# Kernel optimization log

Hardware: AMD Instinct MI355X
Metric: run time of the kernel (lower is better)

Reference implementation:

```python
import jax, jax.numpy as jnp
import numpy as np

DIM = 1024
N_HEADS = 16
HEAD_DIM = DIM // N_HEADS
B, T = 4, 2048


def setup_inputs() -> dict:
    key = jax.random.key(0)
    k_x, k_cos, k_sin, k_wqkv, k_wout = jax.random.split(key, 5)
    x = jax.random.normal(k_x, (B, T, DIM), dtype=jnp.float32)
    # rotary tables indexed by position, half the head dim
    pos = jnp.arange(T, dtype=jnp.float32)[:, None]
    inv_freq = 1.0 / (10000.0 ** (jnp.arange(0, HEAD_DIM, 2, dtype=jnp.float32) / HEAD_DIM))
    ang = pos * inv_freq[None, :]  # [T, HEAD_DIM//2]
    cos = jnp.cos(ang)
    sin = jnp.sin(ang)
    mask = jnp.zeros((T, T), dtype=jnp.float32)
    Wqkv = jax.random.normal(k_wqkv, (3 * DIM, DIM), dtype=jnp.float32) * 0.02
    Wout = jax.random.normal(k_wout, (DIM, DIM), dtype=jnp.float32) * 0.02
    return {"x": x, "cos": cos, "sin": sin, "mask": mask, "Wqkv": Wqkv, "Wout": Wout}


def _apply_rope(t, cos, sin):
    # t: [B, T, H, D]; cos/sin: [T, D//2]
    d = t.shape[-1]
    t1, t2 = t[..., : d // 2], t[..., d // 2 :]
    c = cos[: t.shape[1]][None, :, None, :]
    s = sin[: t.shape[1]][None, :, None, :]
    return jnp.concatenate([t1 * c - t2 * s, t1 * s + t2 * c], axis=-1)


def reference(x, cos, sin, mask, Wqkv, Wout):
    Bx, Tx, C = x.shape
    scale = HEAD_DIM ** -0.5
    qkv = (x @ Wqkv.T).reshape(Bx, Tx, 3, N_HEADS, HEAD_DIM)
    q, k, v = qkv[:, :, 0], qkv[:, :, 1], qkv[:, :, 2]
    q = _apply_rope(q, cos, sin)
    k = _apply_rope(k, cos, sin)
    attn = jnp.einsum("bthd,bshd->bhts", q, k) * scale  # [B, H, T, T]
    attn = attn + mask[None, None, :, :]
    p = jax.nn.softmax(attn, axis=-1)
    out = jnp.einsum("bhts,bshd->bthd", p, v).reshape(Bx, Tx, C)
    return out @ Wout.T
```

## Files before the change

### kernel.cpp

```cpp
#include <hip/hip_runtime.h>
#include <math.h>

#define DIMC   1024
#define NHEADS 16
#define HD     64
#define BATCH  4
#define SEQ    2048
#define MROWS  (BATCH * SEQ)
#define QKVC   (3 * DIMC)
#define QSCALE 0.1803368801111204f

typedef __bf16 bf16x8 __attribute__((ext_vector_type(8)));
typedef float  f32x4  __attribute__((ext_vector_type(4)));
typedef short  s16x4  __attribute__((ext_vector_type(4)));
typedef unsigned short us;

#define MFMA16(a, b, c) __builtin_amdgcn_mfma_f32_16x16x32_bf16(a, b, c, 0, 0, 0)

__device__ __forceinline__ f32x4 mfma16x16x16(s16x4 a, s16x4 b, f32x4 c) {
#if __has_builtin(__builtin_amdgcn_mfma_f32_16x16x16bf16_1k)
    return __builtin_amdgcn_mfma_f32_16x16x16bf16_1k(a, b, c, 0, 0, 0);
#else
    asm volatile("v_mfma_f32_16x16x16_bf16 %0, %1, %2, %0"
                 : "+v"(c) : "v"(a), "v"(b));
    return c;
#endif
}

__device__ __forceinline__ void async16(const void* g, void* l) {
    __builtin_amdgcn_global_load_lds(
        (const __attribute__((address_space(1))) void*)g,
        (__attribute__((address_space(3))) void*)l, 16, 0, 0);
}

__device__ __forceinline__ bf16x8 ldsfrag(const us* p) {
    union { int4 q; bf16x8 v; } u;
    u.q = *(const int4*)p;
    return u.v;
}

__device__ __forceinline__ s16x4 ldsfrag64(const us* p) {
    union { uint2 q; s16x4 v; } u;
    u.q = *(const uint2*)p;
    return u.v;
}

__device__ __forceinline__ bf16x8 gfrag(const us* __restrict__ p) {
    union { int4 q; bf16x8 v; } u;
    u.q = *(const int4*)p;
    return u.v;
}

__device__ __forceinline__ us bf16_rn(float f) {
    unsigned int u = __builtin_bit_cast(unsigned int, f);
    u += 0x7fffu + ((u >> 16) & 1u);
    return (us)(u >> 16);
}

__device__ __forceinline__ float fast_exp2(float x) {
#if __has_builtin(__builtin_amdgcn_exp2f)
    return __builtin_amdgcn_exp2f(x);
#else
    return __expf(x * 0.6931471805599453f);
#endif
}

__device__ __forceinline__ s16x4 pack4t(float a, float b, float c, float d) {
    union { unsigned u[2]; s16x4 v; } z;
    z.u[0] = __builtin_amdgcn_perm(__builtin_bit_cast(unsigned, b),
                                   __builtin_bit_cast(unsigned, a), 0x07060302);
    z.u[1] = __builtin_amdgcn_perm(__builtin_bit_cast(unsigned, d),
                                   __builtin_bit_cast(unsigned, c), 0x07060302);
    return z.v;
}

#define NX (MROWS * DIMC)
#define NW (QKVC * DIMC)
#define NO (DIMC * DIMC)
#define NC (SEQ * 32)
__global__ __launch_bounds__(256) void cast3_bf16(const float* __restrict__ x,
                                                  const float* __restrict__ wq,
                                                  const float* __restrict__ wo,
                                                  const float* __restrict__ cosb,
                                                  const float* __restrict__ sinb,
                                                  us* __restrict__ xb,
                                                  us* __restrict__ wqb,
                                                  us* __restrict__ wob,
                                                  float* __restrict__ cs2) {
    int i = (blockIdx.x * 256 + threadIdx.x) * 4;
    const float* src;
    us* dst;
    if (i < NX)                { src = x  + i;             dst = xb  + i; }
    else if (i < NX + NW)      { src = wq + (i - NX);      dst = wqb + (i - NX); }
    else if (i < NX + NW + NO) { src = wo + (i - NX - NW); dst = wob + (i - NX - NW); }
    else {
        int p0 = i - (NX + NW + NO);
        if (p0 >= NC) return;
        float4 c4 = *(const float4*)(cosb + p0);
        float4 s4 = *(const float4*)(sinb + p0);
        float4 o0 = {c4.x, s4.x, c4.y, s4.y};
        float4 o1 = {c4.z, s4.z, c4.w, s4.w};
        *(float4*)(cs2 + 2 * p0)     = o0;
        *(float4*)(cs2 + 2 * p0 + 4) = o1;
        return;
    }
    float4 v = *(const float4*)src;
    ushort4 o = {bf16_rn(v.x), bf16_rn(v.y), bf16_rn(v.z), bf16_rn(v.w)};
    *(ushort4*)dst = o;
}

template <int MODE, int NCOLS, int NBLK>
__global__ __launch_bounds__(512, 1) void gemm256(const us* __restrict__ A,
                                                  const us* __restrict__ B,
                                                  void* __restrict__ Cv,
                                                  const float* __restrict__ cs2,
                                                  us* __restrict__ vt) {
    __shared__ __align__(16) us As[3][256 * 64];
    __shared__ __align__(16) us Bs[3][128 * 64];

    const int tid  = threadIdx.x;
    const int lane = tid & 63, w = tid >> 6;
    const int col  = lane & 15, quad = lane >> 4;
    const int r8   = lane >> 3, c8 = lane & 7;
    const int wm   = (w >> 1) * 64, wn = (w & 1) * 64;

    const int f    = blockIdx.y * gridDim.x + blockIdx.x;
    const int xcd  = f & 7, idx = f >> 3;
    const int m0   = (xcd * 4 + idx / NBLK) * 256;
    const int n0   = (idx % NBLK) * 128;

    const us* Ag = A + (size_t)(m0 + w * 8 + r8) * 1024 + (c8 ^ r8) * 8;
    const us* Bg = B + (size_t)(n0 + w * 8 + r8) * 1024 + (c8 ^ r8) * 8;
    us* Ad = &As[0][0] + w * 512 + lane * 8;
    us* Bd = &Bs[0][0] + w * 512 + lane * 8;

    auto stage0 = [&](int kt, int bb) __attribute__((always_inline)) {
        const us* ag = Ag + kt * 64;
        us* ad = Ad + bb * (256 * 64);
        async16(ag, ad);
        async16(ag + (size_t)64 * 1024, ad + 4096);
        async16(Bg + kt * 64, Bd + bb * (128 * 64));
    };
    auto stage1 = [&](int kt, int bb) __attribute__((always_inline)) {
        const us* ag = Ag + kt * 64;
        us* ad = Ad + bb * (256 * 64);
        async16(ag + (size_t)128 * 1024, ad + 8192);
        async16(ag + (size_t)192 * 1024, ad + 12288);
        async16(Bg + kt * 64 + (size_t)64 * 1024, Bd + bb * (128 * 64) + 4096);
    };

    f32x4 acc[4][4] = {};

    stage0(0, 0); stage1(0, 0);
    stage0(1, 1); stage1(1, 1);
    asm volatile("s_waitcnt vmcnt(6)" ::: "memory");
    __builtin_amdgcn_s_barrier();
    __builtin_amdgcn_sched_barrier(0);

    const int swz = col & 7;
#pragma unroll
    for (int kt = 0; kt < 16; ++kt) {
        const us* Ab = &As[kt % 3][0];
        const us* Bb = &Bs[kt % 3][0];
        const int nb = (kt + 2) % 3;
        const bool pf = (kt + 2 < 16);

        {
            bf16x8 af[4], bf[4];
#pragma unroll
            for (int mt = 0; mt < 4; ++mt)
                af[mt] = ldsfrag(Ab + (wm + mt * 16 + col) * 64 + ((quad ^ swz) * 8));
#pragma unroll
            for (int nt = 0; nt < 4; ++nt)
                bf[nt] = ldsfrag(Bb + (wn + nt * 16 + col) * 64 + ((quad ^ swz) * 8));
            if (pf) stage0(kt + 2, nb);
            __builtin_amdgcn_s_barrier();
            asm volatile("s_waitcnt lgkmcnt(0)" ::: "memory");
            __builtin_amdgcn_sched_barrier(0);
            __builtin_amdgcn_s_setprio(1);
#pragma unroll
            for (int mt = 0; mt < 4; ++mt)
#pragma unroll
                for (int nt = 0; nt < 4; ++nt)
                    acc[mt][nt] = MFMA16(af[mt], bf[nt], acc[mt][nt]);
            __builtin_amdgcn_s_setprio(0);
            __builtin_amdgcn_s_barrier();
        }
        {
            bf16x8 af[4], bf[4];
#pragma unroll
            for (int mt = 0; mt < 4; ++mt)
                af[mt] = ldsfrag(Ab + (wm + mt * 16 + col) * 64 + (((4 + quad) ^ swz) * 8));
#pragma unroll
            for (int nt = 0; nt < 4; ++nt)
                bf[nt] = ldsfrag(Bb + (wn + nt * 16 + col) * 64 + (((4 + quad) ^ swz) * 8));
            if (pf) stage1(kt + 2, nb);
            __builtin_amdgcn_s_barrier();
            asm volatile("s_waitcnt lgkmcnt(0)" ::: "memory");
            __builtin_amdgcn_sched_barrier(0);
            __builtin_amdgcn_s_setprio(1);
#pragma unroll
            for (int mt = 0; mt < 4; ++mt)
#pragma unroll
                for (int nt = 0; nt < 4; ++nt)
                    acc[mt][nt] = MFMA16(af[mt], bf[nt], acc[mt][nt]);
            __builtin_amdgcn_s_setprio(0);
            if (kt + 2 < 16)
                asm volatile("s_waitcnt vmcnt(6)" ::: "memory");
            else if (kt + 1 < 16)
                asm volatile("s_waitcnt vmcnt(0)" ::: "memory");
            __builtin_amdgcn_s_barrier();
            __builtin_amdgcn_sched_barrier(0);
        }
    }

    if constexpr (MODE == 1) {
        us* C = (us*)Cv;
        const int gcol0 = n0 + wn;
        const bool is_v = (gcol0 >= 2 * DIMC);
        if (is_v) {
            const int hh   = (gcol0 - 2 * DIMC) >> 6;
            const int bidx = (m0 + wm) >> 11;
            const int tb0  = (m0 + wm) & (SEQ - 1);
#pragma unroll
            for (int mt = 0; mt < 4; ++mt) {
                const int tb = tb0 + mt * 16 + quad * 4;
#pragma unroll
                for (int nt = 0; nt < 4; ++nt) {
                    const int d = nt * 16 + col;
                    ushort4 o = {bf16_rn(acc[mt][nt][0]), bf16_rn(acc[mt][nt][1]),
                                 bf16_rn(acc[mt][nt][2]), bf16_rn(acc[mt][nt][3])};
                    *(ushort4*)(vt + ((size_t)((bidx * 16 + hh) * 64 + d)) * SEQ + tb) = o;
                }
            }
        } else {
            const float fq = (gcol0 < DIMC) ? QSCALE : 1.0f;
#pragma unroll
            for (int mt = 0; mt < 4; ++mt) {
#pragma unroll
                for (int r = 0; r < 4; ++r) {
                    const int grow = m0 + wm + mt * 16 + quad * 4 + r;
                    const int t = grow & (SEQ - 1);
#pragma unroll
                    for (int nt = 0; nt < 2; ++nt) {
                        const int d1 = nt * 16 + col;
                        const float2 cs = ((const float2*)cs2)[t * 32 + d1];
                        const float v1 = acc[mt][nt][r];
                        const float v2 = acc[mt][nt + 2][r];
                        C[(size_t)grow * NCOLS + gcol0 + d1]      = bf16_rn((v1 * cs.x - v2 * cs.y) * fq);
                        C[(size_t)grow * NCOLS + gcol0 + d1 + 32] = bf16_rn((v1 * cs.y + v2 * cs.x) * fq);
                    }
                }
            }
        }
    } else {
        float* C = (float*)Cv;
#pragma unroll
        for (int mt = 0; mt < 4; ++mt)
#pragma unroll
            for (int nt = 0; nt < 4; ++nt)
#pragma unroll
                for (int r = 0; r < 4; ++r)
                    C[(size_t)(m0 + wm + mt * 16 + quad * 4 + r) * NCOLS +
                      n0 + wn + nt * 16 + col] = acc[mt][nt][r];
    }
}

__global__ __launch_bounds__(256, 2) void attn_mfma(const us* __restrict__ qkv,
                                                    const us* __restrict__ vt,
                                                    us* __restrict__ outb) {
    __shared__ __align__(16) us Ls[4][8192];

    const int tid  = threadIdx.x;
    const int lane = tid & 63, w = tid >> 6;
    const int col  = lane & 15, quad = lane >> 4;

    const int f  = blockIdx.y * gridDim.x + blockIdx.x;
    const int c  = (f & 7) * 64 + (f >> 3);
    const int bh = c >> 3, b = bh >> 4, h = bh & 15;
    const int t0 = (c & 7) * 256;

    const int r8 = lane >> 3;
    const int cs = ((lane & 7) ^ r8) * 8;

    const int sw0 = ((quad ^ (col & 7)) << 3);
    const int sw4 = sw0 ^ 32;
    const int e2 = quad >> 1, o4 = (quad & 1) * 4, cm = col & 7;

    const us* qb = qkv + (size_t)b * SEQ * QKVC + h * HD;

    bf16x8 aq[4][2];
#pragma unroll
    for (int s = 0; s < 4; ++s)
#pragma unroll
        for (int hf = 0; hf < 2; ++hf)
            aq[s][hf] = gfrag(qb + (size_t)(t0 + s * 64 + w * 16 + col) * QKVC +
                              hf * 32 + quad * 8);

    const us* kg0 = qkv + (size_t)(b * SEQ + r8) * QKVC + DIMC + h * HD + cs;
    const us* vg0 = vt + ((size_t)bh * HD + r8) * SEQ + cs;
    us* kl = &Ls[w][0]    + lane * 8;
    us* vl = &Ls[w][4096] + lane * 8;

    union { us u[4]; s16x4 v; } ones4;
#pragma unroll
    for (int i = 0; i < 4; ++i) ones4.u[i] = 0x3F80;

    f32x4 o_acc[4][4] = {};
    f32x4 lacc[4] = {};

#pragma unroll
    for (int i = 0; i < 8; ++i)
        async16(kg0 + (size_t)(8 * i) * QKVC, kl + 512 * i);
#pragma unroll
    for (int i = 0; i < 8; ++i)
        async16(vg0 + (size_t)(8 * i) * SEQ, vl + 512 * i);
    asm volatile("s_waitcnt vmcnt(0)" ::: "memory");
    __builtin_amdgcn_sched_barrier(0);

    for (int s0 = 0; s0 < SEQ; s0 += 64) {
        const us* Kb = &Ls[w][0];
        const us* Vb = &Ls[w][4096];

        bf16x8 bk[4][2];
        s16x4  bv[4][4];
#pragma unroll
        for (int nt = 0; nt < 4; ++nt) {
            bk[nt][0] = ldsfrag(Kb + (nt * 16 + col) * 64 + sw0);
            bk[nt][1] = ldsfrag(Kb + (nt * 16 + col) * 64 + sw4);
#pragma unroll
            for (int dt = 0; dt < 4; ++dt)
                bv[nt][dt] = ldsfrag64(Vb + (dt * 16 + col) * 64 +
                                       (((nt * 2 + e2) ^ cm) << 3) + o4);
        }
        asm volatile("s_waitcnt lgkmcnt(0)" ::: "memory");
        __builtin_amdgcn_sched_barrier(0);

        if (s0 + 64 < SEQ) {
            const us* kn = kg0 + (size_t)(s0 + 64) * QKVC;
            const us* vn = vg0 + (s0 + 64);
#pragma unroll
            for (int i = 0; i < 8; ++i)
                async16(kn + (size_t)(8 * i) * QKVC, kl + 512 * i);
#pragma unroll
            for (int i = 0; i < 8; ++i)
                async16(vn + (size_t)(8 * i) * SEQ, vl + 512 * i);
        }

#pragma unroll
        for (int s = 0; s < 4; ++s) {
            f32x4 st[4] = {};
            __builtin_amdgcn_s_setprio(1);
#pragma unroll
            for (int nt = 0; nt < 4; ++nt) {
                st[nt] = MFMA16(bk[nt][0], aq[s][0], st[nt]);
                st[nt] = MFMA16(bk[nt][1], aq[s][1], st[nt]);
            }
            __builtin_amdgcn_s_setprio(0);
            s16x4 ap[4];
#pragma unroll
            for (int nt = 0; nt < 4; ++nt)
                ap[nt] = pack4t(fast_exp2(st[nt][0]), fast_exp2(st[nt][1]),
                                fast_exp2(st[nt][2]), fast_exp2(st[nt][3]));
            __builtin_amdgcn_s_setprio(1);
#pragma unroll
            for (int nt = 0; nt < 4; ++nt)
                lacc[s] = mfma16x16x16(ap[nt], ones4.v, lacc[s]);
#pragma unroll
            for (int dt = 0; dt < 4; ++dt)
#pragma unroll
                for (int nt = 0; nt < 4; ++nt)
                    o_acc[s][dt] = mfma16x16x16(ap[nt], bv[nt][dt], o_acc[s][dt]);
            __builtin_amdgcn_s_setprio(0);
        }

        if (s0 + 64 < SEQ) {
            asm volatile("s_waitcnt vmcnt(0)" ::: "memory");
            __builtin_amdgcn_sched_barrier(0);
        }
    }

#pragma unroll
    for (int s = 0; s < 4; ++s) {
        float linv[4];
#pragma unroll
        for (int r = 0; r < 4; ++r) linv[r] = __builtin_amdgcn_rcpf(lacc[s][r]);
#pragma unroll
        for (int dt = 0; dt < 4; ++dt)
#pragma unroll
            for (int r = 0; r < 4; ++r) {
                const int t = t0 + s * 64 + w * 16 + quad * 4 + r;
                const int d = h * HD + dt * 16 + col;
                outb[(size_t)(b * SEQ + t) * DIMC + d] = bf16_rn(o_acc[s][dt][r] * linv[r]);
            }
    }
}

extern "C" void kernel_launch(void* const* d_in, const int* in_sizes, int n_in,
                              void* d_out, int out_size, void* d_ws, size_t ws_size,
                              hipStream_t stream) {
    const float* x    = (const float*)d_in[0];
    const float* cosb = (const float*)d_in[1];
    const float* sinb = (const float*)d_in[2];
    const float* Wqkv = (const float*)d_in[4];
    const float* Wout = (const float*)d_in[5];
    float* out = (float*)d_out;

    us* xb    = (us*)d_ws;
    us* wqkb  = xb + (size_t)MROWS * DIMC;
    us* woutb = wqkb + (size_t)QKVC * DIMC;
    us* qkvb  = woutb + (size_t)DIMC * DIMC;
    us* vtb   = qkvb + (size_t)MROWS * QKVC;
    us* aob   = vtb + (size_t)BATCH * NHEADS * HD * SEQ;
    float* cs2 = (float*)(aob + (size_t)MROWS * DIMC);

    cast3_bf16<<<(NX + NW + NO + NC) / 1024, 256, 0, stream>>>(
        x, Wqkv, Wout, cosb, sinb, xb, wqkb, woutb, cs2);

    gemm256<1, QKVC, QKVC / 128><<<dim3(QKVC / 128, MROWS / 256), 512, 0, stream>>>(
        xb, wqkb, qkvb, cs2, vtb);

    attn_mfma<<<dim3(SEQ / 256, BATCH * NHEADS), 256, 0, stream>>>(qkvb, vtb, aob);

    gemm256<0, DIMC, DIMC / 128><<<dim3(DIMC / 128, MROWS / 256), 512, 0, stream>>>(
        aob, woutb, out, nullptr, nullptr);
}
```

Baseline: 293.2 us.

## Use 16x16x32 MFMA for PV via permlane swaps of probability fragments

Replaces the 16x16x16 bf16 MFMAs for the P·V product and row-sum with 16x16x32 MFMAs, halving the MFMA count there. The exp'd score fragments are rearranged across lanes with v_permlane32_swap/permlane16_swap so they match the K=32 A-operand layout, and V is loaded as 128-bit LDS fragments instead of 64-bit ones. This adds cross-lane permute instructions and changes the V swizzle indexing, with some risk to layout correctness.

```diff
diff --git a/kernel.cpp b/kernel.cpp
--- a/kernel.cpp
+++ b/kernel.cpp
@@ -17,16 +17,6 @@
 
 #define MFMA16(a, b, c) __builtin_amdgcn_mfma_f32_16x16x32_bf16(a, b, c, 0, 0, 0)
 
-__device__ __forceinline__ f32x4 mfma16x16x16(s16x4 a, s16x4 b, f32x4 c) {
-#if __has_builtin(__builtin_amdgcn_mfma_f32_16x16x16bf16_1k)
-    return __builtin_amdgcn_mfma_f32_16x16x16bf16_1k(a, b, c, 0, 0, 0);
-#else
-    asm volatile("v_mfma_f32_16x16x16_bf16 %0, %1, %2, %0"
-                 : "+v"(c) : "v"(a), "v"(b));
-    return c;
-#endif
-}
-
 __device__ __forceinline__ void async16(const void* g, void* l) {
     __builtin_amdgcn_global_load_lds(
         (const __attribute__((address_space(1))) void*)g,
@@ -36,12 +26,6 @@
 __device__ __forceinline__ bf16x8 ldsfrag(const us* p) {
     union { int4 q; bf16x8 v; } u;
     u.q = *(const int4*)p;
-    return u.v;
-}
-
-__device__ __forceinline__ s16x4 ldsfrag64(const us* p) {
-    union { uint2 q; s16x4 v; } u;
-    u.q = *(const uint2*)p;
     return u.v;
 }
 
@@ -65,13 +49,9 @@
 #endif
 }
 
-__device__ __forceinline__ s16x4 pack4t(float a, float b, float c, float d) {
-    union { unsigned u[2]; s16x4 v; } z;
-    z.u[0] = __builtin_amdgcn_perm(__builtin_bit_cast(unsigned, b),
-                                   __builtin_bit_cast(unsigned, a), 0x07060302);
-    z.u[1] = __builtin_amdgcn_perm(__builtin_bit_cast(unsigned, d),
-                                   __builtin_bit_cast(unsigned, c), 0x07060302);
-    return z.v;
+__device__ __forceinline__ unsigned pack2t(float a, float b) {
+    return __builtin_amdgcn_perm(__builtin_bit_cast(unsigned, b),
+                                 __builtin_bit_cast(unsigned, a), 0x07060302);
 }
 
 #define NX (MROWS * DIMC)
@@ -285,7 +265,7 @@
 
     const int sw0 = ((quad ^ (col & 7)) << 3);
     const int sw4 = sw0 ^ 32;
-    const int e2 = quad >> 1, o4 = (quad & 1) * 4, cm = col & 7;
+    const int cm = col & 7;
 
     const us* qb = qkv + (size_t)b * SEQ * QKVC + h * HD;
 
@@ -302,9 +282,9 @@
     us* kl = &Ls[w][0]    + lane * 8;
     us* vl = &Ls[w][4096] + lane * 8;
 
-    union { us u[4]; s16x4 v; } ones4;
-#pragma unroll
-    for (int i = 0; i < 4; ++i) ones4.u[i] = 0x3F80;
+    union { us u[8]; bf16x8 v; } ones8;
+#pragma unroll
+    for (int i = 0; i < 8; ++i) ones8.u[i] = 0x3F80;
 
     f32x4 o_acc[4][4] = {};
     f32x4 lacc[4] = {};
@@ -323,16 +303,18 @@
         const us* Vb = &Ls[w][4096];
 
         bf16x8 bk[4][2];
-        s16x4  bv[4][4];
+        bf16x8 bv[4][2];
 #pragma unroll
         for (int nt = 0; nt < 4; ++nt) {
             bk[nt][0] = ldsfrag(Kb + (nt * 16 + col) * 64 + sw0);
             bk[nt][1] = ldsfrag(Kb + (nt * 16 + col) * 64 + sw4);
-#pragma unroll
-            for (int dt = 0; dt < 4; ++dt)
-                bv[nt][dt] = ldsfrag64(Vb + (dt * 16 + col) * 64 +
-                                       (((nt * 2 + e2) ^ cm) << 3) + o4);
-        }
+        }
+#pragma unroll
+        for (int dt = 0; dt < 4; ++dt)
+#pragma unroll
+            for (int cc = 0; cc < 2; ++cc)
+                bv[dt][cc] = ldsfrag(Vb + (dt * 16 + col) * 64 +
+                                     (((4 * cc + quad) ^ cm) << 3));
         asm volatile("s_waitcnt lgkmcnt(0)" ::: "memory");
         __builtin_amdgcn_sched_barrier(0);
 
@@ -357,21 +339,32 @@
                 st[nt] = MFMA16(bk[nt][1], aq[s][1], st[nt]);
             }
             __builtin_amdgcn_s_setprio(0);
-            s16x4 ap[4];
-#pragma unroll
-            for (int nt = 0; nt < 4; ++nt)
-                ap[nt] = pack4t(fast_exp2(st[nt][0]), fast_exp2(st[nt][1]),
-                                fast_exp2(st[nt][2]), fast_exp2(st[nt][3]));
-            __builtin_amdgcn_s_setprio(1);
-#pragma unroll
-            for (int nt = 0; nt < 4; ++nt)
-                lacc[s] = mfma16x16x16(ap[nt], ones4.v, lacc[s]);
-#pragma unroll
-            for (int dt = 0; dt < 4; ++dt)
-#pragma unroll
-                for (int nt = 0; nt < 4; ++nt)
-                    o_acc[s][dt] = mfma16x16x16(ap[nt], bv[nt][dt], o_acc[s][dt]);
-            __builtin_amdgcn_s_setprio(0);
+            unsigned wlo[4], whi[4];
+#pragma unroll
+            for (int nt = 0; nt < 4; ++nt) {
+                wlo[nt] = pack2t(fast_exp2(st[nt][0]), fast_exp2(st[nt][1]));
+                whi[nt] = pack2t(fast_exp2(st[nt][2]), fast_exp2(st[nt][3]));
+            }
+#pragma unroll
+            for (int cc = 0; cc < 2; ++cc) {
+                unsigned a0 = wlo[2 * cc], b0 = wlo[2 * cc + 1];
+                unsigned a1 = whi[2 * cc], b1 = whi[2 * cc + 1];
+                asm volatile("v_permlane32_swap_b32 %0, %1" : "+v"(a0), "+v"(b0));
+                asm volatile("v_permlane16_swap_b32 %0, %1" : "+v"(a0), "+v"(b0));
+                asm volatile("v_permlane32_swap_b32 %0, %1" : "+v"(a1), "+v"(b1));
+                asm volatile("v_permlane16_swap_b32 %0, %1" : "+v"(a1), "+v"(b1));
+                union { unsigned u[4]; bf16x8 v; } af;
+                af.u[0] = a0;
+                af.u[1] = a1;
+                af.u[2] = b0;
+                af.u[3] = b1;
+                __builtin_amdgcn_s_setprio(1);
+                lacc[s] = MFMA16(af.v, ones8.v, lacc[s]);
+#pragma unroll
+                for (int dt = 0; dt < 4; ++dt)
+                    o_acc[s][dt] = MFMA16(af.v, bv[dt][cc], o_acc[s][dt]);
+                __builtin_amdgcn_s_setprio(0);
+            }
         }
 
         if (s0 + 64 < SEQ) {
```

Measured after the change: 278.1 us. 1.05x faster.
